# Performance work log

Hardware: AMD Instinct MI355X
Metric: run time of the kernel (lower is better)

Reference implementation:

```python
import jax, jax.numpy as jnp
import numpy as np

I, H, O, L = 128, 1024, 128, 2

def _linear_init(key, out_f, in_f, bias):
    b = 1.0 / np.sqrt(in_f)
    kw, kb = jax.random.split(key)
    W = jax.random.uniform(kw, (out_f, in_f), jnp.float32, -b, b)
    if bias:
        return W, jax.random.uniform(kb, (out_f,), jnp.float32, -b, b)
    return W, None

def setup_inputs() -> dict:
    key = jax.random.key(0)
    ks = jax.random.split(key, 32)
    inp = {
        'x': jax.random.normal(ks[0], (32, 512, I), jnp.float32),
        'h0': jnp.zeros((32, L, H), jnp.float32),
    }
    ki = 1
    in_dim = I
    for l in range(L):
        Wxz, _ = _linear_init(ks[ki], H, in_dim, False); ki += 1
        Whz, bz = _linear_init(ks[ki], H, H, True); ki += 1
        Wxr, _ = _linear_init(ks[ki], H, in_dim, False); ki += 1
        Whr, br = _linear_init(ks[ki], H, H, True); ki += 1
        Wxg, _ = _linear_init(ks[ki], H, in_dim, False); ki += 1
        Whg, bg = _linear_init(ks[ki], H, H, True); ki += 1
        inp.update({f'Wxz{l}': Wxz, f'Whz{l}': Whz, f'bz{l}': bz,
                    f'Wxr{l}': Wxr, f'Whr{l}': Whr, f'br{l}': br,
                    f'Wxg{l}': Wxg, f'Whg{l}': Whg, f'bg{l}': bg})
        in_dim = H
    Wy, by = _linear_init(ks[ki], O, H, True)
    inp['Wy'] = Wy
    inp['by'] = by
    return inp

def _gru_layer(x_seq, h0, Wxz, Whz, bz, Wxr, Whr, br, Wxg, Whg, bg):
    # Precompute all input projections as big GEMMs (B,S,H)
    xz = jnp.einsum('bsi,hi->bsh', x_seq, Wxz)
    xr = jnp.einsum('bsi,hi->bsh', x_seq, Wxr)
    xg = jnp.einsum('bsi,hi->bsh', x_seq, Wxg)
    def step(h, gates):
        gz, gr, gg = gates
        z = jax.nn.sigmoid(gz + h @ Whz.T + bz)
        r = jax.nn.sigmoid(gr + h @ Whr.T + br)
        g = jnp.tanh(gg + (r * h) @ Whg.T + bg)
        h_new = z * h + (1.0 - z) * g
        return h_new, h_new
    # scan over time: (S,B,H)
    hT, hs = jax.lax.scan(step, h0, (xz.transpose(1, 0, 2), xr.transpose(1, 0, 2), xg.transpose(1, 0, 2)))
    return hs.transpose(1, 0, 2), hT

def reference(x, h0,
              Wxz0, Whz0, bz0, Wxr0, Whr0, br0, Wxg0, Whg0, bg0,
              Wxz1, Whz1, bz1, Wxr1, Whr1, br1, Wxg1, Whg1, bg1,
              Wy, by):
    layers = [
        (Wxz0, Whz0, bz0, Wxr0, Whr0, br0, Wxg0, Whg0, bg0),
        (Wxz1, Whz1, bz1, Wxr1, Whr1, br1, Wxg1, Whg1, bg1),
    ]
    seq = x
    finals = []
    for l, p in enumerate(layers):
        seq, hT = _gru_layer(seq, h0[:, l, :], *p)
        finals.append(hT)
    y = jnp.einsum('bsh,oh->bso', seq, Wy) + by  # (B,S,O)
    hidden = jnp.stack(finals, axis=1)  # (B,L,H)
    return y, hidden
```

## Files before the change

kernel.cpp:

```cpp
#include <hip/hip_runtime.h>

typedef unsigned short u16;
typedef unsigned int u32;
typedef unsigned long long u64;
typedef __bf16 bf16x8 __attribute__((ext_vector_type(8)));
typedef float f32x4 __attribute__((ext_vector_type(4)));

union FU { f32x4 f; bf16x8 h; };

__device__ __forceinline__ u16 f2b(float f) {
  unsigned u = __float_as_uint(f);
  return (u16)((u + 0x7fffu + ((u >> 16) & 1u)) >> 16);
}

__device__ __forceinline__ void st_b16_llc(u16* p, u16 v) {
  __hip_atomic_store(p, v, __ATOMIC_RELAXED, __HIP_MEMORY_SCOPE_AGENT);
}

__device__ __forceinline__ void st_u32_cc(u32* p, u32 v) {
  asm volatile("global_store_dword %0, %1, off sc0 sc1" :: "v"(p), "v"(v) : "memory");
}
__device__ __forceinline__ void st_u64_cc(void* p, u64 v) {
  asm volatile("global_store_dwordx2 %0, %1, off sc0 sc1" :: "v"(p), "v"(v) : "memory");
}

__device__ __forceinline__ u32 ld_dword_cc(const u32* p) {
  u32 v;
  asm volatile("global_load_dword %0, %1, off sc0 sc1\n\ts_waitcnt vmcnt(0)"
               : "=v"(v) : "v"(p) : "memory");
  return v;
}

__device__ __forceinline__ u64 pack4(u32 lo) {
  u32 p2 = lo | ((u32)__shfl_xor((int)lo, 1) << 16);
  return (u64)p2 | ((u64)(u32)__shfl_xor((int)p2, 2) << 32);
}

#define ISSUE8CC(D, P)                                                       \
  asm volatile(                                                              \
      "global_load_dwordx4 %0, %8, off sc0 sc1\n\t"                          \
      "global_load_dwordx4 %1, %8, off offset:64 sc0 sc1\n\t"                \
      "global_load_dwordx4 %2, %8, off offset:128 sc0 sc1\n\t"               \
      "global_load_dwordx4 %3, %8, off offset:192 sc0 sc1\n\t"               \
      "global_load_dwordx4 %4, %8, off offset:256 sc0 sc1\n\t"               \
      "global_load_dwordx4 %5, %8, off offset:320 sc0 sc1\n\t"               \
      "global_load_dwordx4 %6, %8, off offset:384 sc0 sc1\n\t"               \
      "global_load_dwordx4 %7, %8, off offset:448 sc0 sc1"                   \
      : "=&v"((D)[0].f), "=&v"((D)[1].f), "=&v"((D)[2].f), "=&v"((D)[3].f),  \
        "=&v"((D)[4].f), "=&v"((D)[5].f), "=&v"((D)[6].f), "=&v"((D)[7].f)   \
      : "v"(P) : "memory")

#define ISSUE4C(D, P)                                                        \
  asm volatile(                                                              \
      "global_load_dwordx4 %0, %4, off\n\t"                                  \
      "global_load_dwordx4 %1, %4, off offset:64\n\t"                        \
      "global_load_dwordx4 %2, %4, off offset:128\n\t"                       \
      "global_load_dwordx4 %3, %4, off offset:192"                           \
      : "=&v"((D)[0].f), "=&v"((D)[1].f), "=&v"((D)[2].f), "=&v"((D)[3].f)   \
      : "v"(P) : "memory")

#define WAITV(N)                                                             \
  do {                                                                       \
    asm volatile("s_waitcnt vmcnt(" #N ")" ::: "memory");                    \
    __builtin_amdgcn_sched_barrier(0);                                       \
  } while (0)

#define MFMA8ZR(ACC, BUF, KSB)                                               \
  do {                                                                       \
    _Pragma("unroll") for (int j_ = 0; j_ < 8; ++j_)                         \
        ACC = __builtin_amdgcn_mfma_f32_16x16x32_bf16(                       \
            (BUF)[j_].h,                                                     \
            *(const bf16x8*)&zr_frag[(KSB + j_) * 512 + lane * 8],           \
            ACC, 0, 0, 0);                                                   \
  } while (0)
#define MFMA8G(ACC, BUF, KSB)                                                \
  do {                                                                       \
    _Pragma("unroll") for (int j_ = 0; j_ < 8; ++j_)                         \
        ACC = __builtin_amdgcn_mfma_f32_16x16x32_bf16(                       \
            (BUF)[j_].h,                                                     \
            *(const bf16x8*)&g_frag[(KSB + j_) * 256 + boff],                \
            ACC, 0, 0, 0);                                                   \
  } while (0)

__global__ void cast_f32_bf16(const float* __restrict__ in, u16* __restrict__ out, int n) {
  int i = blockIdx.x * 256 + threadIdx.x;
  if (i < n) out[i] = f2b(in[i]);
}

__global__ __launch_bounds__(256) void gemm_bt(
    const u16* __restrict__ A, const u16* __restrict__ B,
    int M, int N, int K,
    const float* __restrict__ bias, float* __restrict__ Cf)
{
  __shared__ u16 a_sm[128 * 32];
  __shared__ u16 b_sm[128 * 32];
  const int tid = threadIdx.x;
  const int lane = tid & 63;
  const int wid = tid >> 6;
  const int wm = wid >> 1, wn = wid & 1;
  const int m0 = blockIdx.x * 128, n0 = blockIdx.y * 128;
  const int q = lane >> 4, l15 = lane & 15, l3 = lane & 3;

  f32x4 acc[4][4];
  #pragma unroll
  for (int i = 0; i < 4; ++i)
    #pragma unroll
    for (int j = 0; j < 4; ++j) acc[i][j] = (f32x4){0.f, 0.f, 0.f, 0.f};

  for (int kk = 0; kk < K; kk += 32) {
    __syncthreads();
    #pragma unroll
    for (int p = 0; p < 2; ++p) {
      int idx = p * 256 + tid;
      int r = idx >> 2, cch = idx & 3;
      *(uint4*)&a_sm[r * 32 + ((cch ^ (r & 3)) * 8)] =
          *(const uint4*)&A[(size_t)(m0 + r) * K + kk + cch * 8];
      *(uint4*)&b_sm[r * 32 + ((cch ^ (r & 3)) * 8)] =
          *(const uint4*)&B[(size_t)(n0 + r) * K + kk + cch * 8];
    }
    __syncthreads();
    bf16x8 af[4], bfr[4];
    #pragma unroll
    for (int s = 0; s < 4; ++s) {
      int ra = wm * 64 + s * 16 + l15;
      af[s] = *(const bf16x8*)&a_sm[ra * 32 + ((q ^ l3) * 8)];
      int rb = wn * 64 + s * 16 + l15;
      bfr[s] = *(const bf16x8*)&b_sm[rb * 32 + ((q ^ l3) * 8)];
    }
    #pragma unroll
    for (int si = 0; si < 4; ++si)
      #pragma unroll
      for (int sj = 0; sj < 4; ++sj)
        acc[si][sj] = __builtin_amdgcn_mfma_f32_16x16x32_bf16(af[si], bfr[sj], acc[si][sj], 0, 0, 0);
  }

  #pragma unroll
  for (int si = 0; si < 4; ++si)
    #pragma unroll
    for (int sj = 0; sj < 4; ++sj)
      #pragma unroll
      for (int e = 0; e < 4; ++e) {
        int m = m0 + wm * 64 + si * 16 + q * 4 + e;
        int n = n0 + wn * 64 + sj * 16 + l15;
        Cf[(size_t)m * N + n] = acc[si][sj][e] + (bias ? bias[n] : 0.f);
      }
}

__global__ __launch_bounds__(192, 1) void gru_pipe(
    const u16* __restrict__ Wh0, const u16* __restrict__ Wx0,
    const u16* __restrict__ Wh1, const u16* __restrict__ Wx1,
    const float* __restrict__ bz0, const float* __restrict__ br0, const float* __restrict__ bg0,
    const float* __restrict__ bz1, const float* __restrict__ br1, const float* __restrict__ bg1,
    const u16* __restrict__ xb,
    const float* __restrict__ h0p,
    u16* __restrict__ h0buf,
    u16* __restrict__ hb1,
    u16* __restrict__ rh0b, u16* __restrict__ rh1b,
    u16* __restrict__ seq1,
    float* __restrict__ hid,
    u32* __restrict__ slots)
{
  __shared__ u16 zr_frag[64 * 512];
  __shared__ u16 g_frag[64 * 256];

  const int tid = threadIdx.x;
  const int lane = tid & 63;
  const int w = tid >> 6;
  const int bid = blockIdx.x;
  u32* lflags = slots + 512;

  const bool Lyr1 = bid >= 128;
  const int nb = (bid & 127) * 8;
  const int q = lane >> 4, c15 = lane & 15, nl = c15 & 7;
  const int n_own = nb + nl;
  const bool isz = c15 < 8;
  const int brow = w * 16 + c15;
  const int boff = (q * 8 + nl) * 8;
  const int aoff = brow * 1024 + q * 8;
  const int KS = Lyr1 ? 64 : 36;
  const int IN = Lyr1 ? 1024 : 128;
  const u16* Wh = Lyr1 ? Wh1 : Wh0;
  const u16* Wx = Lyr1 ? Wx1 : Wx0;
  const size_t WXG = (size_t)1024 * IN;

  const int d_own = (Lyr1 ? 2 : 0) | (w & 1);
  const int d_oth = (Lyr1 ? 0 : 2) | (w & 1);
  u32* slot_ptr = &slots[d_own * 128 + (bid & 127)];
  const int rrep = bid >> 5;
  const bool laneOth = (lane & 1) != 0;
  const u32* lfp = &lflags[rrep * 32 + (laneOth ? d_oth : d_own)];

  float hreg[4], zreg[4] = {0.f, 0.f, 0.f, 0.f};
  f32x4 a1g = {0.f, 0.f, 0.f, 0.f};

  if (tid < 128) {
    for (int cidx = tid; cidx < KS * 64; cidx += 128) {
      int ks = cidx >> 6, l = cidx & 63;
      int lq = l >> 4, lc = l & 15;
      int row = nb + (lc & 7), gate = (lc < 8) ? 0 : 1;
      int k0 = ks * 32 + lq * 8;
      const u16* src = (k0 < 1024)
          ? Wh + (size_t)gate * 1048576 + (size_t)row * 1024 + k0
          : Wx + (size_t)gate * WXG + (size_t)row * IN + (k0 - 1024);
      *(uint4*)&zr_frag[cidx * 8] = *(const uint4*)src;
    }
    for (int gidx = tid; gidx < KS * 32; gidx += 128) {
      int ks = gidx >> 5, s = gidx & 31;
      int lq = s >> 3, r8 = s & 7;
      int row = nb + r8, k0 = ks * 32 + lq * 8;
      const u16* src = (k0 < 1024)
          ? Wh + (size_t)2 * 1048576 + (size_t)row * 1024 + k0
          : Wx + (size_t)2 * WXG + (size_t)row * IN + (k0 - 1024);
      *(uint4*)&g_frag[gidx * 8] = *(const uint4*)src;
    }
    #pragma unroll
    for (int e = 0; e < 4; ++e) {
      int b = w * 16 + q * 4 + e;
      float v = h0p[b * 2048 + (Lyr1 ? 1024 : 0) + n_own];
      hreg[e] = v;
      if (isz)
        st_b16_llc((Lyr1 ? hb1 : h0buf + 32768) + b * 1024 + n_own, f2b(v));
    }
  }
  __syncthreads();

  if (w == 2) {
    if (bid == 0) {
      const u32* my = slots + lane * 8;
      const int dgrp = lane >> 4;
      u32 pub = 0;
      for (;;) {
        uint4 va, vb;
        asm volatile(
            "global_load_dwordx4 %0, %2, off sc0 sc1\n\t"
            "global_load_dwordx4 %1, %2, off offset:16 sc0 sc1\n\t"
            "s_waitcnt vmcnt(0)"
            : "=&v"(va), "=&v"(vb) : "v"(my) : "memory");
        u32 m = min(min(min(va.x, va.y), min(va.z, va.w)),
                    min(min(vb.x, vb.y), min(vb.z, vb.w)));
        m = min(m, (u32)__shfl_xor((int)m, 1));
        m = min(m, (u32)__shfl_xor((int)m, 2));
        m = min(m, (u32)__shfl_xor((int)m, 4));
        m = min(m, (u32)__shfl_xor((int)m, 8));
        if (m > pub) {
          pub = m;
          if ((lane & 15) == 0) {
            #pragma unroll
            for (int r = 0; r < 8; ++r) st_u32_cc(&lflags[r * 32 + dgrp], m);
          }
        }
        if (__all(pub >= 1026u)) break;
        __builtin_amdgcn_s_sleep(1);
      }
    }
    return;
  }

  if (lane == 0) st_u32_cc(slot_ptr, 1u);

  const float bias1 = isz ? (Lyr1 ? bz1 : bz0)[n_own] : (Lyr1 ? br1 : br0)[n_own];
  const float bias2 = (Lyr1 ? bg1 : bg0)[n_own];

  FU xfu[4];
  FU sA[8], sB[8], sC[8];

  for (int p = 0; p < 1026; ++p) {
    const int t = p >> 1, ph = p & 1;

    {
      const u32 tgt = laneOth ? ((Lyr1 && ph == 0) ? (u32)(p + 1) : (u32)p)
                              : (u32)(p + 1);
      for (;;) {
        u32 v = ld_dword_cc(lfp);
        if (__all(v >= tgt)) break;
        __builtin_amdgcn_s_sleep(1);
      }
    }

    if (!Lyr1) {
      if (t < 512) {
        f32x4 a0 = {0.f,0.f,0.f,0.f}, a1 = {0.f,0.f,0.f,0.f};
        if (ph == 0) {
          const u16* hp = h0buf + ((t - 1) & 1) * 32768 + aoff;
          const u16* xp = xb + ((size_t)brow * 512 + t) * 128 + q * 8;
          ISSUE4C(xfu, xp);
          ISSUE8CC(sA, hp);
          ISSUE8CC(sB, hp + 256);
          ISSUE8CC(sC, hp + 512);
          WAITV(16); MFMA8ZR(a0, sA, 0);
          ISSUE8CC(sA, hp + 768);
          WAITV(16); MFMA8ZR(a0, sB, 8);
          WAITV(8);  MFMA8ZR(a0, sC, 16);
          WAITV(0);  MFMA8ZR(a0, sA, 24);
          #pragma unroll
          for (int j = 0; j < 4; ++j)
            a1 = __builtin_amdgcn_mfma_f32_16x16x32_bf16(
                xfu[j].h, *(const bf16x8*)&zr_frag[(32 + j) * 512 + lane * 8], a1, 0, 0, 0);
          float hsh[4];
          #pragma unroll
          for (int e = 0; e < 4; ++e) hsh[e] = __shfl_xor(hreg[e], 8);
          #pragma unroll
          for (int e = 0; e < 4; ++e) {
            float pre = a0[e] + a1[e] + bias1;
            float s = 1.f / (1.f + __expf(-pre));
            if (isz) zreg[e] = s;
            else {
              u64 p4 = pack4((u32)f2b(s * hsh[e]));
              if ((c15 & 3) == 0)
                st_u64_cc(&rh0b[(w * 16 + q * 4 + e) * 1024 + nb + (c15 & 7)], p4);
            }
          }
        } else {
          const u16* rp = rh0b + aoff;
          ISSUE8CC(sA, rp);
          ISSUE8CC(sB, rp + 256);
          ISSUE8CC(sC, rp + 512);
          WAITV(16); MFMA8G(a0, sA, 0);
          ISSUE8CC(sA, rp + 768);
          WAITV(16); MFMA8G(a0, sB, 8);
          WAITV(8);  MFMA8G(a0, sC, 16);
          WAITV(0);  MFMA8G(a0, sA, 24);
          #pragma unroll
          for (int j = 0; j < 4; ++j)
            a1 = __builtin_amdgcn_mfma_f32_16x16x32_bf16(
                xfu[j].h, *(const bf16x8*)&g_frag[(32 + j) * 256 + boff], a1, 0, 0, 0);
          if (isz) {
            u16* hout = h0buf + (t & 1) * 32768;
            #pragma unroll
            for (int e = 0; e < 4; ++e) {
              int b = w * 16 + q * 4 + e;
              float pre = a0[e] + a1[e] + bias2;
              float ex = __expf(2.f * pre);
              float gv = 1.f - 2.f / (ex + 1.f);
              float hn = zreg[e] * hreg[e] + (1.f - zreg[e]) * gv;
              hreg[e] = hn;
              u64 p4 = pack4((u32)f2b(hn));
              if ((c15 & 3) == 0) st_u64_cc(&hout[b * 1024 + nb + c15], p4);
              if (t == 511) hid[b * 2048 + n_own] = hn;
            }
          }
        }
      }
    } else {
      if (t >= 1) {
        const int s = t - 1;
        f32x4 a0 = {0.f,0.f,0.f,0.f}, a1 = {0.f,0.f,0.f,0.f};
        if (ph == 0) {
          const u16* hp = h0buf + (s & 1) * 32768 + aoff;
          const u16* hb = hb1 + aoff;
          a1g = (f32x4){0.f, 0.f, 0.f, 0.f};
          ISSUE8CC(sA, hb);
          ISSUE8CC(sB, hb + 256);
          ISSUE8CC(sC, hb + 512);
          WAITV(16); MFMA8ZR(a0, sA, 0);  ISSUE8CC(sA, hb + 768);
          WAITV(16); MFMA8ZR(a0, sB, 8);  ISSUE8CC(sB, hp);
          WAITV(16); MFMA8ZR(a0, sC, 16); ISSUE8CC(sC, hp + 256);
          WAITV(16); MFMA8ZR(a0, sA, 24); ISSUE8CC(sA, hp + 512);
          WAITV(16); MFMA8ZR(a1, sB, 32); MFMA8G(a1g, sB, 32);
                     ISSUE8CC(sB, hp + 768);
          WAITV(16); MFMA8ZR(a1, sC, 40); MFMA8G(a1g, sC, 40);
          WAITV(8);  MFMA8ZR(a1, sA, 48); MFMA8G(a1g, sA, 48);
          WAITV(0);  MFMA8ZR(a1, sB, 56); MFMA8G(a1g, sB, 56);
          float hsh[4];
          #pragma unroll
          for (int e = 0; e < 4; ++e) hsh[e] = __shfl_xor(hreg[e], 8);
          #pragma unroll
          for (int e = 0; e < 4; ++e) {
            float pre = a0[e] + a1[e] + bias1;
            float sg = 1.f / (1.f + __expf(-pre));
            if (isz) zreg[e] = sg;
            else {
              u64 p4 = pack4((u32)f2b(sg * hsh[e]));
              if ((c15 & 3) == 0)
                st_u64_cc(&rh1b[(w * 16 + q * 4 + e) * 1024 + nb + (c15 & 7)], p4);
            }
          }
        } else {
          const u16* rp = rh1b + aoff;
          ISSUE8CC(sA, rp);
          ISSUE8CC(sB, rp + 256);
          ISSUE8CC(sC, rp + 512);
          WAITV(16); MFMA8G(a0, sA, 0);
          ISSUE8CC(sA, rp + 768);
          WAITV(16); MFMA8G(a0, sB, 8);
          WAITV(8);  MFMA8G(a0, sC, 16);
          WAITV(0);  MFMA8G(a0, sA, 24);
          if (isz) {
            #pragma unroll
            for (int e = 0; e < 4; ++e) {
              int b = w * 16 + q * 4 + e;
              float pre = a0[e] + a1g[e] + bias2;
              float ex = __expf(2.f * pre);
              float gv = 1.f - 2.f / (ex + 1.f);
              float hn = zreg[e] * hreg[e] + (1.f - zreg[e]) * gv;
              hreg[e] = hn;
              u64 p4 = pack4((u32)f2b(hn));
              if ((c15 & 3) == 0) {
                st_u64_cc(&hb1[b * 1024 + nb + c15], p4);
                *(u64*)&seq1[((size_t)b * 512 + s) * 1024 + nb + c15] = p4;
              }
              if (s == 511) hid[1024 + b * 2048 + n_own] = hn;
            }
          }
        }
      }
    }

    if (p < 1025) {
      WAITV(0);
      if (lane == 0) st_u32_cc(slot_ptr, (u32)(p + 2));
    }
  }
}

extern "C" void kernel_launch(void* const* d_in, const int* in_sizes, int n_in,
                              void* d_out, int out_size, void* d_ws, size_t ws_size,
                              hipStream_t stream) {
  (void)in_sizes; (void)n_in; (void)out_size; (void)ws_size;
  char* ws = (char*)d_ws;
  const size_t MB = 1024ull * 1024ull;
  u16* seq1 = (u16*)(ws + 0);
  u16* xb   = (u16*)(ws + 32 * MB);
  u16* Wh0  = (u16*)(ws + 36 * MB);
  u16* Wh1  = (u16*)(ws + 42 * MB);
  u16* Wx0  = (u16*)(ws + 48 * MB);
  u16* Wx1  = (u16*)(ws + 49 * MB);
  u16* Wyb  = (u16*)(ws + 55 * MB);
  u16* h0buf = (u16*)(ws + 56 * MB);
  u16* hb1  = (u16*)(ws + 56 * MB + 128 * 1024);
  u16* rh0b = (u16*)(ws + 56 * MB + 192 * 1024);
  u16* rh1b = (u16*)(ws + 56 * MB + 256 * 1024);
  u32* slots = (u32*)(ws + 56 * MB + 320 * 1024);

  hipMemsetAsync(slots, 0, 4096, stream);

  auto cast = [&](const void* in, u16* out, int n) {
    cast_f32_bf16<<<(n + 255) / 256, 256, 0, stream>>>((const float*)in, out, n);
  };
  cast(d_in[0], xb, 2097152);
  cast(d_in[3],  Wh0 + 0,       1048576);
  cast(d_in[6],  Wh0 + 1048576, 1048576);
  cast(d_in[9],  Wh0 + 2097152, 1048576);
  cast(d_in[12], Wh1 + 0,       1048576);
  cast(d_in[15], Wh1 + 1048576, 1048576);
  cast(d_in[18], Wh1 + 2097152, 1048576);
  cast(d_in[2],  Wx0 + 0,      131072);
  cast(d_in[5],  Wx0 + 131072, 131072);
  cast(d_in[8],  Wx0 + 262144, 131072);
  cast(d_in[11], Wx1 + 0,       1048576);
  cast(d_in[14], Wx1 + 1048576, 1048576);
  cast(d_in[17], Wx1 + 2097152, 1048576);
  cast(d_in[20], Wyb, 131072);

  float* y_out = (float*)d_out;
  float* hid = y_out + 2097152;

  gru_pipe<<<256, dim3(192), 0, stream>>>(
      Wh0, Wx0, Wh1, Wx1,
      (const float*)d_in[4],  (const float*)d_in[7],  (const float*)d_in[10],
      (const float*)d_in[13], (const float*)d_in[16], (const float*)d_in[19],
      xb, (const float*)d_in[1],
      h0buf, hb1, rh0b, rh1b, seq1, hid, slots);

  gemm_bt<<<dim3(128, 1), dim3(256), 0, stream>>>(
      seq1, Wyb, 16384, 128, 1024, (const float*)d_in[21], y_out);
}
```

Before: 6.117 ms.

## Replace central flag-relay wave with direct per-wave polling of all slots

Removes the dedicated third wave in block 0 that reduced the per-block progress slots and republished them as aggregated flags. Each compute wave now polls the 128 producer slots of its own and the other layer directly, using dwordx4 loads spread over 32 lanes per half-wave and a wave-wide min check. This cuts one relay hop from every step's dependency chain, and the block size drops to 128 threads. The layer-1 seq1 output store is also deferred until after the progress flag is published, taking it off the critical signalling path. The cost is much more polling traffic hitting the shared slot lines from every wave.

```diff
diff --git a/kernel.cpp b/kernel.cpp
--- a/kernel.cpp
+++ b/kernel.cpp
@@ -24,9 +24,9 @@
   asm volatile("global_store_dwordx2 %0, %1, off sc0 sc1" :: "v"(p), "v"(v) : "memory");
 }
 
-__device__ __forceinline__ u32 ld_dword_cc(const u32* p) {
-  u32 v;
-  asm volatile("global_load_dword %0, %1, off sc0 sc1\n\ts_waitcnt vmcnt(0)"
+__device__ __forceinline__ uint4 ld_poll4(const u32* p) {
+  uint4 v;
+  asm volatile("global_load_dwordx4 %0, %1, off sc0 sc1\n\ts_waitcnt vmcnt(0)"
                : "=v"(v) : "v"(p) : "memory");
   return v;
 }
@@ -146,7 +146,7 @@
       }
 }
 
-__global__ __launch_bounds__(192, 1) void gru_pipe(
+__global__ __launch_bounds__(128, 1) void gru_pipe(
     const u16* __restrict__ Wh0, const u16* __restrict__ Wx0,
     const u16* __restrict__ Wh1, const u16* __restrict__ Wx1,
     const float* __restrict__ bz0, const float* __restrict__ br0, const float* __restrict__ bg0,
@@ -167,7 +167,6 @@
   const int lane = tid & 63;
   const int w = tid >> 6;
   const int bid = blockIdx.x;
-  u32* lflags = slots + 512;
 
   const bool Lyr1 = bid >= 128;
   const int nb = (bid & 127) * 8;
@@ -183,79 +182,44 @@
   const u16* Wx = Lyr1 ? Wx1 : Wx0;
   const size_t WXG = (size_t)1024 * IN;
 
-  const int d_own = (Lyr1 ? 2 : 0) | (w & 1);
-  const int d_oth = (Lyr1 ? 0 : 2) | (w & 1);
+  const int d_own = (Lyr1 ? 2 : 0) | w;
+  const int d_oth = (Lyr1 ? 0 : 2) | w;
   u32* slot_ptr = &slots[d_own * 128 + (bid & 127)];
-  const int rrep = bid >> 5;
-  const bool laneOth = (lane & 1) != 0;
-  const u32* lfp = &lflags[rrep * 32 + (laneOth ? d_oth : d_own)];
+  const int othHalf = lane >> 5;
+  const u32* pollp = &slots[(othHalf ? d_oth : d_own) * 128 + (lane & 31) * 4];
 
   float hreg[4], zreg[4] = {0.f, 0.f, 0.f, 0.f};
   f32x4 a1g = {0.f, 0.f, 0.f, 0.f};
-
-  if (tid < 128) {
-    for (int cidx = tid; cidx < KS * 64; cidx += 128) {
-      int ks = cidx >> 6, l = cidx & 63;
-      int lq = l >> 4, lc = l & 15;
-      int row = nb + (lc & 7), gate = (lc < 8) ? 0 : 1;
-      int k0 = ks * 32 + lq * 8;
-      const u16* src = (k0 < 1024)
-          ? Wh + (size_t)gate * 1048576 + (size_t)row * 1024 + k0
-          : Wx + (size_t)gate * WXG + (size_t)row * IN + (k0 - 1024);
-      *(uint4*)&zr_frag[cidx * 8] = *(const uint4*)src;
-    }
-    for (int gidx = tid; gidx < KS * 32; gidx += 128) {
-      int ks = gidx >> 5, s = gidx & 31;
-      int lq = s >> 3, r8 = s & 7;
-      int row = nb + r8, k0 = ks * 32 + lq * 8;
-      const u16* src = (k0 < 1024)
-          ? Wh + (size_t)2 * 1048576 + (size_t)row * 1024 + k0
-          : Wx + (size_t)2 * WXG + (size_t)row * IN + (k0 - 1024);
-      *(uint4*)&g_frag[gidx * 8] = *(const uint4*)src;
-    }
-    #pragma unroll
-    for (int e = 0; e < 4; ++e) {
-      int b = w * 16 + q * 4 + e;
-      float v = h0p[b * 2048 + (Lyr1 ? 1024 : 0) + n_own];
-      hreg[e] = v;
-      if (isz)
-        st_b16_llc((Lyr1 ? hb1 : h0buf + 32768) + b * 1024 + n_own, f2b(v));
-    }
+  u64 p4s[4];
+
+  for (int cidx = tid; cidx < KS * 64; cidx += 128) {
+    int ks = cidx >> 6, l = cidx & 63;
+    int lq = l >> 4, lc = l & 15;
+    int row = nb + (lc & 7), gate = (lc < 8) ? 0 : 1;
+    int k0 = ks * 32 + lq * 8;
+    const u16* src = (k0 < 1024)
+        ? Wh + (size_t)gate * 1048576 + (size_t)row * 1024 + k0
+        : Wx + (size_t)gate * WXG + (size_t)row * IN + (k0 - 1024);
+    *(uint4*)&zr_frag[cidx * 8] = *(const uint4*)src;
+  }
+  for (int gidx = tid; gidx < KS * 32; gidx += 128) {
+    int ks = gidx >> 5, s = gidx & 31;
+    int lq = s >> 3, r8 = s & 7;
+    int row = nb + r8, k0 = ks * 32 + lq * 8;
+    const u16* src = (k0 < 1024)
+        ? Wh + (size_t)2 * 1048576 + (size_t)row * 1024 + k0
+        : Wx + (size_t)2 * WXG + (size_t)row * IN + (k0 - 1024);
+    *(uint4*)&g_frag[gidx * 8] = *(const uint4*)src;
+  }
+  #pragma unroll
+  for (int e = 0; e < 4; ++e) {
+    int b = w * 16 + q * 4 + e;
+    float v = h0p[b * 2048 + (Lyr1 ? 1024 : 0) + n_own];
+    hreg[e] = v;
+    if (isz)
+      st_b16_llc((Lyr1 ? hb1 : h0buf + 32768) + b * 1024 + n_own, f2b(v));
   }
   __syncthreads();
-
-  if (w == 2) {
-    if (bid == 0) {
-      const u32* my = slots + lane * 8;
-      const int dgrp = lane >> 4;
-      u32 pub = 0;
-      for (;;) {
-        uint4 va, vb;
-        asm volatile(
-            "global_load_dwordx4 %0, %2, off sc0 sc1\n\t"
-            "global_load_dwordx4 %1, %2, off offset:16 sc0 sc1\n\t"
-            "s_waitcnt vmcnt(0)"
-            : "=&v"(va), "=&v"(vb) : "v"(my) : "memory");
-        u32 m = min(min(min(va.x, va.y), min(va.z, va.w)),
-                    min(min(vb.x, vb.y), min(vb.z, vb.w)));
-        m = min(m, (u32)__shfl_xor((int)m, 1));
-        m = min(m, (u32)__shfl_xor((int)m, 2));
-        m = min(m, (u32)__shfl_xor((int)m, 4));
-        m = min(m, (u32)__shfl_xor((int)m, 8));
-        if (m > pub) {
-          pub = m;
-          if ((lane & 15) == 0) {
-            #pragma unroll
-            for (int r = 0; r < 8; ++r) st_u32_cc(&lflags[r * 32 + dgrp], m);
-          }
-        }
-        if (__all(pub >= 1026u)) break;
-        __builtin_amdgcn_s_sleep(1);
-      }
-    }
-    return;
-  }
-
   if (lane == 0) st_u32_cc(slot_ptr, 1u);
 
   const float bias1 = isz ? (Lyr1 ? bz1 : bz0)[n_own] : (Lyr1 ? br1 : br0)[n_own];
@@ -268,11 +232,12 @@
     const int t = p >> 1, ph = p & 1;
 
     {
-      const u32 tgt = laneOth ? ((Lyr1 && ph == 0) ? (u32)(p + 1) : (u32)p)
+      const u32 tgt = othHalf ? ((Lyr1 && ph == 0) ? (u32)(p + 1) : (u32)p)
                               : (u32)(p + 1);
       for (;;) {
-        u32 v = ld_dword_cc(lfp);
-        if (__all(v >= tgt)) break;
+        uint4 v = ld_poll4(pollp);
+        u32 m = min(min(v.x, v.y), min(v.z, v.w));
+        if (__all(m >= tgt)) break;
         __builtin_amdgcn_s_sleep(1);
       }
     }
@@ -395,10 +360,8 @@
               float hn = zreg[e] * hreg[e] + (1.f - zreg[e]) * gv;
               hreg[e] = hn;
               u64 p4 = pack4((u32)f2b(hn));
-              if ((c15 & 3) == 0) {
-                st_u64_cc(&hb1[b * 1024 + nb + c15], p4);
-                *(u64*)&seq1[((size_t)b * 512 + s) * 1024 + nb + c15] = p4;
-              }
+              p4s[e] = p4;
+              if ((c15 & 3) == 0) st_u64_cc(&hb1[b * 1024 + nb + c15], p4);
               if (s == 511) hid[1024 + b * 2048 + n_own] = hn;
             }
           }
@@ -409,6 +372,11 @@
     if (p < 1025) {
       WAITV(0);
       if (lane == 0) st_u32_cc(slot_ptr, (u32)(p + 2));
+    }
+    if (Lyr1 && ph == 1 && t >= 1 && isz && (c15 & 3) == 0) {
+      #pragma unroll
+      for (int e = 0; e < 4; ++e)
+        *(u64*)&seq1[((size_t)(w * 16 + q * 4 + e) * 512 + (t - 1)) * 1024 + nb + c15] = p4s[e];
     }
   }
 }
@@ -455,7 +423,7 @@
   float* y_out = (float*)d_out;
   float* hid = y_out + 2097152;
 
-  gru_pipe<<<256, dim3(192), 0, stream>>>(
+  gru_pipe<<<256, dim3(128), 0, stream>>>(
       Wh0, Wx0, Wh1, Wx1,
       (const float*)d_in[4],  (const float*)d_in[7],  (const float*)d_in[10],
       (const float*)d_in[13], (const float*)d_in[16], (const float*)d_in[19],
```

New measurement: 9.048 ms. 47.9% more time.
